# Kernel tuning notes

Measured on AMD Instinct MI355X. Metric: run time of the kernel, lower is better.

Reference implementation:

```python
import jax, jax.numpy as jnp
import numpy as np

B, S, E, D, DE = 8, 128, 50, 300, 50  # batch, seq, edge_dim, gcn_dim, dep_embed_dim
EPS = 1e-6


def setup_inputs() -> dict:
    key = jax.random.key(0)
    ks = jax.random.split(key, 9)
    weight_prob_softmax = jax.nn.softmax(jax.random.normal(ks[0], (B, S, S, E)), axis=2)
    weight_adj = jax.random.normal(ks[1], (B, S, S, E))
    gcn_inputs = jax.random.normal(ks[2], (B, S, D))
    # self-loop added to adjacency after permute -> [B, E, S, S]; identity loops
    self_loop = jnp.broadcast_to(jnp.eye(S, dtype=jnp.float32), (B, E, S, S))
    W_w = jax.random.normal(ks[3], (D, D)) * 0.05          # gcn linear (in, out)
    W_b = jnp.zeros((D,))
    ln_a = jnp.ones((D,))
    ln_b = jnp.zeros((D,))
    refine_W = jax.random.normal(ks[4], (2 * D + 3 * E, DE)) * 0.05  # (750, 50)
    refine_b = jnp.zeros((DE,))
    return {
        "weight_prob_softmax": weight_prob_softmax,
        "weight_adj": weight_adj,
        "gcn_inputs": gcn_inputs,
        "self_loop": self_loop,
        "W_w": W_w, "W_b": W_b,
        "ln_a": ln_a, "ln_b": ln_b,
        "refine_W": refine_W, "refine_b": refine_b,
    }


def reference(weight_prob_softmax, weight_adj, gcn_inputs, self_loop,
              W_w, W_b, ln_a, ln_b, refine_W, refine_b):
    b, s, d = gcn_inputs.shape
    e = weight_prob_softmax.shape[-1]
    # [B,S,S,E] -> [B,E,S,S], add self loops
    wps = jnp.transpose(weight_prob_softmax, (0, 3, 1, 2)) + self_loop
    # per-relation-channel message passing: Ax[b,e,i,:] = sum_j wps[b,e,i,j] * x[b,j,:]
    Ax = jnp.einsum('beij,bjd->beid', wps, gcn_inputs)
    Ax = Ax.mean(axis=1)  # avg pooling over edge channels -> [B,S,D]
    h = Ax @ W_w + W_b
    # LayerNorm with unbiased std (torch x.std default) and (std + eps)
    mean = h.mean(axis=-1, keepdims=True)
    var_unbiased = jnp.sum((h - mean) ** 2, axis=-1, keepdims=True) / (d - 1)
    std = jnp.sqrt(var_unbiased)
    h = ln_a * (h - mean) / (std + EPS) + ln_b
    node = jax.nn.relu(h)  # [B,S,D]
    # node1[b,i,j] = node[b,j]; node2[b,i,j] = node[b,i]
    node1 = jnp.broadcast_to(node[:, None, :, :], (b, s, s, d))
    node2 = jnp.broadcast_to(node[:, :, None, :], (b, s, s, d))
    # diagonal edge features: [B,E,S] -> [B,S,E]
    diag = jnp.transpose(jnp.diagonal(weight_adj, axis1=1, axis2=2), (0, 2, 1))
    edge_i = jnp.broadcast_to(diag[:, None, :, :], (b, s, s, e))  # edge_i[b,i,j]=diag[b,j]
    edge_j = jnp.broadcast_to(diag[:, :, None, :], (b, s, s, e))  # edge_j[b,i,j]=diag[b,i]
    feat = jnp.concatenate([weight_adj, edge_i, edge_j, node1, node2], axis=-1)
    edge_out = feat @ refine_W + refine_b  # [B,S,S,DE]
    return node, edge_out
```

## Files before the change

kernel.cpp:

```cpp
#include <hip/hip_runtime.h>
#include <hip/hip_bf16.h>


typedef __bf16 bf16x8 __attribute__((ext_vector_type(8)));
typedef float f32x4 __attribute__((ext_vector_type(4)));

__device__ __forceinline__ unsigned short f2bf(float f) {
    __hip_bfloat16 h = __float2bfloat16(f);
    union { __hip_bfloat16 h; unsigned short u; } c; c.h = h; return c.u;
}

__global__ void __launch_bounds__(320) k_xw(
    const float* __restrict__ x, const float* __restrict__ Ww,
    float* __restrict__ XW)
{
    __shared__ __align__(16) float xr[304];
    int tid = threadIdx.x;
    int row = blockIdx.x;
    if (tid < 300) xr[tid] = x[(size_t)row * 300 + tid];
    else if (tid < 304) xr[tid] = 0.f;
    __syncthreads();
    if (tid < 300) {
        const float* wp = Ww + tid;
        const f32x4* x4 = (const f32x4*)xr;
        float acc = 0.f;
#pragma unroll 5
        for (int k4 = 0; k4 < 75; ++k4) {
            f32x4 xv = x4[k4];
            int k = k4 * 4;
            acc += xv[0] * wp[(k + 0) * 300];
            acc += xv[1] * wp[(k + 1) * 300];
            acc += xv[2] * wp[(k + 2) * 300];
            acc += xv[3] * wp[(k + 3) * 300];
        }
        XW[(size_t)row * 300 + tid] = acc;
    }
}

__global__ void __launch_bounds__(256) k_node(
    const float* __restrict__ wps,
    const float* __restrict__ wa,
    const float* __restrict__ XW,
    const float* __restrict__ Wb,
    const float* __restrict__ lna,
    const float* __restrict__ lnb,
    const float* __restrict__ Rw,
    const float* __restrict__ rb,
    float* __restrict__ node_out,
    float* __restrict__ R1, float* __restrict__ R2)
{
    __shared__ __align__(16) float stage[6400];
    __shared__ float Ml[128];
    __shared__ float srcL[352];
    __shared__ float p1s[5][50], p2s[5][50];
    __shared__ float red[8];
    __shared__ float stats[2];
    int tid = threadIdx.x;
    int row = blockIdx.x;
    int b = row >> 7, i = row & 127;

    const float4* w4 = (const float4*)(wps + (size_t)row * 6400);
    float4* s4 = (float4*)stage;
    for (int t = tid; t < 1600; t += 256) s4[t] = w4[t];
    if (tid < 50) srcL[tid] = wa[((size_t)row * 128 + i) * 50 + tid];
    if (tid >= 350 - 256 && tid < 96) {}
    __syncthreads();

    if (tid < 128) {
        const float* p = stage + tid * 50;
        float s = 0.f;
#pragma unroll
        for (int e = 0; e < 50; ++e) s += p[e];
        Ml[tid] = s * (1.0f / 50.0f) + ((tid == i) ? 1.0f : 0.0f);
    }
    __syncthreads();

    int d0 = tid;
    bool has2 = (tid < 44);
    int d1 = has2 ? 256 + tid : 299;
    float h0 = Wb[d0];
    float h1 = Wb[d1];
    {
        const float* xp = XW + (size_t)b * 38400;
#pragma unroll 16
        for (int j = 0; j < 128; ++j) {
            float m = Ml[j];
            h0 += m * xp[j * 300 + d0];
            h1 += m * xp[j * 300 + d1];
        }
    }

    {
        float s1 = h0 + (has2 ? h1 : 0.f);
        float s2 = h0 * h0 + (has2 ? h1 * h1 : 0.f);
        for (int off = 32; off > 0; off >>= 1) {
            s1 += __shfl_down(s1, off);
            s2 += __shfl_down(s2, off);
        }
        int wv = tid >> 6, lane = tid & 63;
        if (lane == 0) { red[wv] = s1; red[4 + wv] = s2; }
    }
    __syncthreads();
    if (tid == 0) {
        float s1 = red[0] + red[1] + red[2] + red[3];
        float s2 = red[4] + red[5] + red[6] + red[7];
        float mean = s1 * (1.0f / 300.0f);
        float var = (s2 - 300.0f * mean * mean) * (1.0f / 299.0f);
        var = fmaxf(var, 0.0f);
        stats[0] = mean;
        stats[1] = 1.0f / (sqrtf(var) + 1e-6f);
    }
    __syncthreads();

    {
        float mean = stats[0], inv = stats[1];
        float n0 = fmaxf(lna[d0] * (h0 - mean) * inv + lnb[d0], 0.f);
        node_out[(size_t)row * 300 + d0] = n0;
        srcL[50 + d0] = n0;
        if (has2) {
            float n1 = fmaxf(lna[d1] * (h1 - mean) * inv + lnb[d1], 0.f);
            node_out[(size_t)row * 300 + d1] = n1;
            srcL[50 + d1] = n1;
        }
    }
    __syncthreads();

    if (tid < 250) {
        int p = tid / 50, k = tid % 50;
        int srcOff, w1b, w2b, len;
        if (p == 0) { srcOff = 0;  w1b = 50 * 50;  w2b = 100 * 50; len = 50; }
        else {
            int dd = (p - 1) * 75;
            srcOff = 50 + dd; w1b = (150 + dd) * 50; w2b = (450 + dd) * 50; len = 75;
        }
        float r1 = 0.f, r2 = 0.f;
        const float* w1p = Rw + w1b + k;
        const float* w2p = Rw + w2b + k;
#pragma unroll 5
        for (int t = 0; t < len; ++t) {
            float sv = srcL[srcOff + t];
            r1 += sv * w1p[t * 50];
            r2 += sv * w2p[t * 50];
        }
        p1s[p][k] = r1; p2s[p][k] = r2;
    }
    __syncthreads();
    if (tid < 50) {
        float s1 = 0.f, s2 = rb[tid];
#pragma unroll
        for (int p = 0; p < 5; ++p) { s1 += p1s[p][tid]; s2 += p2s[p][tid]; }
        R1[(size_t)row * 50 + tid] = s1;
        R2[(size_t)row * 50 + tid] = s2;
    }
}

__global__ void __launch_bounds__(256) k_edge(
    const float* __restrict__ wa,
    const float* __restrict__ Rw,
    const float* __restrict__ R1, const float* __restrict__ R2,
    float* __restrict__ eout)
{
    __shared__ __align__(16) unsigned char smem[27648];
    unsigned short* waA  = (unsigned short*)smem;
    unsigned short* rwBT = (unsigned short*)(smem + 18432);
    float* outF = (float*)smem;
    int tid = threadIdx.x;
    int bi = blockIdx.x;
    int b = bi >> 7;

    for (int idx = tid; idx < 2304; idx += 256) ((unsigned int*)rwBT)[idx] = 0u;
    for (int idx = tid; idx < 1408; idx += 256) {
        int j = idx / 11, c = idx % 11;
        *((unsigned int*)(waA + j * 72 + 50) + c) = 0u;
    }
    __syncthreads();

    const float2* wap = (const float2*)(wa + (size_t)bi * 6400);
    for (int idx = tid; idx < 3200; idx += 256) {
        float2 v = wap[idx];
        int f = idx * 2;
        int j = f / 50, e = f % 50;
        unsigned int pack = (unsigned int)f2bf(v.x) | ((unsigned int)f2bf(v.y) << 16);
        *(unsigned int*)(waA + j * 72 + e) = pack;
    }
    for (int idx = tid; idx < 2500; idx += 256) {
        int e = idx / 50, kk = idx % 50;
        rwBT[kk * 72 + e] = f2bf(Rw[idx]);
    }
    __syncthreads();

    int lane = tid & 63, wv = tid >> 6;
    int q = lane >> 4, lr = lane & 15;
    f32x4 acc[2][4] = {};

#pragma unroll
    for (int ks = 0; ks < 2; ++ks) {
        int e0 = ks * 32 + q * 8;
        bf16x8 a0 = *(const bf16x8*)&waA[(wv * 32 + lr) * 72 + e0];
        bf16x8 a1 = *(const bf16x8*)&waA[(wv * 32 + 16 + lr) * 72 + e0];
#pragma unroll
        for (int nt = 0; nt < 4; ++nt) {
            bf16x8 bb = *(const bf16x8*)&rwBT[(nt * 16 + lr) * 72 + e0];
            acc[0][nt] = __builtin_amdgcn_mfma_f32_16x16x32_bf16(a0, bb, acc[0][nt], 0, 0, 0);
            acc[1][nt] = __builtin_amdgcn_mfma_f32_16x16x32_bf16(a1, bb, acc[1][nt], 0, 0, 0);
        }
    }
    __syncthreads();

    const float* r2p = R2 + (size_t)bi * 50;
#pragma unroll
    for (int nt = 0; nt < 4; ++nt) {
        int kk = nt * 16 + lr;
        if (kk < 50) {
            float r2v = r2p[kk];
#pragma unroll
            for (int mi = 0; mi < 2; ++mi) {
                int jbase = wv * 32 + mi * 16 + q * 4;
#pragma unroll
                for (int r = 0; r < 4; ++r)
                    outF[(jbase + r) * 50 + kk] = acc[mi][nt][r] + r2v;
            }
        }
    }
    __syncthreads();

    const float4* R1b = (const float4*)(R1 + (size_t)b * 6400);
    const float4* L4  = (const float4*)outF;
    float4* op4 = (float4*)(eout + (size_t)bi * 6400);
    for (int f4 = tid; f4 < 1600; f4 += 256) {
        float4 v = L4[f4];
        float4 r = R1b[f4];
        v.x += r.x; v.y += r.y; v.z += r.z; v.w += r.w;
        op4[f4] = v;
    }
}

extern "C" void kernel_launch(void* const* d_in, const int* in_sizes, int n_in,
                              void* d_out, int out_size, void* d_ws, size_t ws_size,
                              hipStream_t stream)
{
    const float* wps = (const float*)d_in[0];
    const float* wa  = (const float*)d_in[1];
    const float* x   = (const float*)d_in[2];
    const float* Ww  = (const float*)d_in[4];
    const float* Wb  = (const float*)d_in[5];
    const float* lna = (const float*)d_in[6];
    const float* lnb = (const float*)d_in[7];
    const float* Rw  = (const float*)d_in[8];
    const float* rb  = (const float*)d_in[9];

    float* R1 = (float*)d_ws;
    float* R2 = ((float*)d_ws) + 51200;

    float* node_out = (float*)d_out;
    float* edge_out = node_out + 307200;
    float* XW = edge_out;

    k_xw  <<<1024, 320, 0, stream>>>(x, Ww, XW);
    k_node<<<1024, 256, 0, stream>>>(wps, wa, XW, Wb, lna, lnb, Rw, rb,
                                     node_out, R1, R2);
    k_edge<<<1024, 256, 0, stream>>>(wa, Rw, R1, R2, edge_out);
}
```

Before: 166.5 us.

## Fuse XW projection into node kernel by reassociating matmul order

Drops the separate x·W kernel and instead computes (M·x)·W inside the node kernel. Each row first aggregates raw inputs with the averaged adjacency row into shared memory, then multiplies by W. This removes one kernel launch and the intermediate XW write and read. The cost is a 300x300 matvec per row inside the node kernel plus an extra barrier. The per-row work is about the same as the old k_xw, now serialized after the aggregation.

```diff
diff --git a/kernel.cpp b/kernel.cpp
--- a/kernel.cpp
+++ b/kernel.cpp
@@ -10,37 +10,11 @@
     union { __hip_bfloat16 h; unsigned short u; } c; c.h = h; return c.u;
 }
 
-__global__ void __launch_bounds__(320) k_xw(
-    const float* __restrict__ x, const float* __restrict__ Ww,
-    float* __restrict__ XW)
-{
-    __shared__ __align__(16) float xr[304];
-    int tid = threadIdx.x;
-    int row = blockIdx.x;
-    if (tid < 300) xr[tid] = x[(size_t)row * 300 + tid];
-    else if (tid < 304) xr[tid] = 0.f;
-    __syncthreads();
-    if (tid < 300) {
-        const float* wp = Ww + tid;
-        const f32x4* x4 = (const f32x4*)xr;
-        float acc = 0.f;
-#pragma unroll 5
-        for (int k4 = 0; k4 < 75; ++k4) {
-            f32x4 xv = x4[k4];
-            int k = k4 * 4;
-            acc += xv[0] * wp[(k + 0) * 300];
-            acc += xv[1] * wp[(k + 1) * 300];
-            acc += xv[2] * wp[(k + 2) * 300];
-            acc += xv[3] * wp[(k + 3) * 300];
-        }
-        XW[(size_t)row * 300 + tid] = acc;
-    }
-}
-
 __global__ void __launch_bounds__(256) k_node(
     const float* __restrict__ wps,
     const float* __restrict__ wa,
-    const float* __restrict__ XW,
+    const float* __restrict__ x,
+    const float* __restrict__ Ww,
     const float* __restrict__ Wb,
     const float* __restrict__ lna,
     const float* __restrict__ lnb,
@@ -51,6 +25,7 @@
 {
     __shared__ __align__(16) float stage[6400];
     __shared__ float Ml[128];
+    __shared__ float axm[304];
     __shared__ float srcL[352];
     __shared__ float p1s[5][50], p2s[5][50];
     __shared__ float red[8];
@@ -63,7 +38,6 @@
     float4* s4 = (float4*)stage;
     for (int t = tid; t < 1600; t += 256) s4[t] = w4[t];
     if (tid < 50) srcL[tid] = wa[((size_t)row * 128 + i) * 50 + tid];
-    if (tid >= 350 - 256 && tid < 96) {}
     __syncthreads();
 
     if (tid < 128) {
@@ -78,15 +52,38 @@
     int d0 = tid;
     bool has2 = (tid < 44);
     int d1 = has2 ? 256 + tid : 299;
-    float h0 = Wb[d0];
-    float h1 = Wb[d1];
-    {
-        const float* xp = XW + (size_t)b * 38400;
+    {
+        float a0 = 0.f, a1 = 0.f;
+        const float* xp = x + (size_t)b * 38400;
 #pragma unroll 16
         for (int j = 0; j < 128; ++j) {
             float m = Ml[j];
-            h0 += m * xp[j * 300 + d0];
-            h1 += m * xp[j * 300 + d1];
+            a0 += m * xp[j * 300 + d0];
+            a1 += m * xp[j * 300 + d1];
+        }
+        axm[d0] = a0;
+        if (has2) axm[d1] = a1;
+    }
+    __syncthreads();
+
+    float h0 = Wb[d0];
+    float h1 = Wb[d1];
+    {
+        const float* wp0 = Ww + d0;
+        const float* wp1 = Ww + d1;
+        const f32x4* a4 = (const f32x4*)axm;
+#pragma unroll 5
+        for (int k4 = 0; k4 < 75; ++k4) {
+            f32x4 av = a4[k4];
+            int k = k4 * 4;
+            h0 += av[0] * wp0[(k + 0) * 300];
+            h0 += av[1] * wp0[(k + 1) * 300];
+            h0 += av[2] * wp0[(k + 2) * 300];
+            h0 += av[3] * wp0[(k + 3) * 300];
+            h1 += av[0] * wp1[(k + 0) * 300];
+            h1 += av[1] * wp1[(k + 1) * 300];
+            h1 += av[2] * wp1[(k + 2) * 300];
+            h1 += av[3] * wp1[(k + 3) * 300];
         }
     }
 
@@ -254,10 +251,8 @@
 
     float* node_out = (float*)d_out;
     float* edge_out = node_out + 307200;
-    float* XW = edge_out;
-
-    k_xw  <<<1024, 320, 0, stream>>>(x, Ww, XW);
-    k_node<<<1024, 256, 0, stream>>>(wps, wa, XW, Wb, lna, lnb, Rw, rb,
+
+    k_node<<<1024, 256, 0, stream>>>(wps, wa, x, Ww, Wb, lna, lnb, Rw, rb,
                                      node_out, R1, R2);
     k_edge<<<1024, 256, 0, stream>>>(wa, Rw, R1, R2, edge_out);
 }
```

Result: no change. 165.2 us (-0.8%).
